# Kernel tuning notes

Hardware: AMD Instinct MI355X
Metric: run time of the kernel (lower is better)

Reference implementation:

```python
import jax, jax.numpy as jnp
import numpy as np
import math

POOL = 7          # RoIAlign output_size
SR = 2            # sampling_ratio


def _roi_align(feat, boxes, bidx):
    """torchvision RoIAlign, aligned=False, spatial_scale=1.0, sampling_ratio=2.
    feat: [B,C,H,W]; boxes: [N,4] (x1,y1,x2,y2) in pixel coords of this level;
    bidx: [N] int batch indices. Returns [N,C,POOL,POOL]."""
    B, C, H, W = feat.shape
    x1, y1, x2, y2 = boxes[:, 0], boxes[:, 1], boxes[:, 2], boxes[:, 3]
    roi_w = jnp.maximum(x2 - x1, 1.0)
    roi_h = jnp.maximum(y2 - y1, 1.0)
    bin_w = roi_w / POOL
    bin_h = roi_h / POOL
    # sample-point offsets within the ROI, in bin units: [POOL, SR]
    off = jnp.arange(POOL, dtype=feat.dtype)[:, None] + (jnp.arange(SR, dtype=feat.dtype)[None, :] + 0.5) / SR
    ys = y1[:, None, None] + bin_h[:, None, None] * off  # [N,POOL,SR]
    xs = x1[:, None, None] + bin_w[:, None, None] * off  # [N,POOL,SR]

    def prep(c, size):
        valid = (c > -1.0) & (c < size)
        c = jnp.clip(c, 0.0, size - 1)
        lo = jnp.floor(c).astype(jnp.int32)
        hi = jnp.minimum(lo + 1, size - 1)
        return lo, hi, c - lo, valid

    y_lo, y_hi, fy, vy = prep(ys, H)
    x_lo, x_hi, fx, vx = prep(xs, W)

    b = bidx.astype(jnp.int32)[:, None, None, None, None]  # [N,1,1,1,1]

    def gather(yi, xi):
        # -> [N,POOL,SR,POOL,SR,C] (advanced indices broadcast, channel slice last)
        return feat[b, :, yi[:, :, :, None, None], xi[:, None, None, :, :]]

    hy = (1.0 - fy)[:, :, :, None, None, None]
    ly = fy[:, :, :, None, None, None]
    hx = (1.0 - fx)[:, None, None, :, :, None]
    lx = fx[:, None, None, :, :, None]
    v = (gather(y_lo, x_lo) * hy * hx + gather(y_lo, x_hi) * hy * lx
         + gather(y_hi, x_lo) * ly * hx + gather(y_hi, x_hi) * ly * lx)
    valid = (vy[:, :, :, None, None] & vx[:, None, None, :, :])[..., None]
    v = jnp.where(valid, v, 0.0)
    out = v.mean(axis=(2, 4))          # average over SRxSR samples -> [N,POOL,POOL,C]
    return out.transpose(0, 3, 1, 2)   # [N,C,POOL,POOL]


def setup_inputs() -> dict:
    key = jax.random.key(0)
    k2, k3, k4, k5, kxy, kwh, kbi = jax.random.split(key, 7)
    N = 1000
    p2 = jax.random.normal(k2, (2, 256, 256, 256), dtype=jnp.float32)
    p3 = jax.random.normal(k3, (2, 256, 128, 128), dtype=jnp.float32)
    p4 = jax.random.normal(k4, (2, 256, 64, 64), dtype=jnp.float32)
    p5 = jax.random.normal(k5, (2, 256, 32, 32), dtype=jnp.float32)
    xy = jax.random.uniform(kxy, (N, 2), minval=0.0, maxval=0.7)
    wh = jax.random.uniform(kwh, (N, 2), minval=0.02, maxval=0.3)
    rpn_bbox = jnp.concatenate([xy, xy + wh], axis=1)  # (x1,y1,x2,y2) normalized
    box_index = jax.random.randint(kbi, (N,), 0, 2, dtype=jnp.int32)
    return {"p2": p2, "p3": p3, "p4": p4, "p5": p5,
            "rpn_bbox": rpn_bbox, "box_index": box_index}


def reference(p2, p3, p4, p5, rpn_bbox, box_index):
    feats = [p2, p3, p4, p5]
    N = rpn_bbox.shape[0]
    x1, y1, x2, y2 = rpn_bbox[:, 0], rpn_bbox[:, 1], rpn_bbox[:, 2], rpn_bbox[:, 3]
    area = (y2 - y1) * (x2 - x1)
    roi_level = jnp.log(jnp.sqrt(area)) / math.log(2.0)
    roi_level = jnp.clip(jnp.round(roi_level) + 4.0, 0.0, 3.0).astype(jnp.int32)
    # Compute RoIAlign of every ROI at every level, then select per-ROI level.
    # (The masked-select / per-level dispatch / argsort-combine in the original
    # restores original ROI order, so this is mathematically identical.)
    pooled_per_level = jnp.stack(
        [_roi_align(f, rpn_bbox * f.shape[3], box_index) for f in feats], axis=0
    )  # [4, N, C, 7, 7]
    pooled = pooled_per_level[roi_level, jnp.arange(N)]  # [N, C, 7, 7]
    return pooled
```

## Files before the change

### kernel.cpp

```cpp
#include <hip/hip_runtime.h>
#include <math.h>

#define POOL 7
#define NCELL 49
#define NCH 256
#define CH_SPLIT 8
#define CHPB (NCH / CH_SPLIT)
#define CHPW (CHPB / 4)
#define LDSF 640
#define NIT 10

typedef __attribute__((address_space(1))) void global_void;
typedef __attribute__((address_space(3))) void lds_void;
__device__ __forceinline__ void async_stage(const float* g, float* l) {
    __builtin_amdgcn_global_load_lds((global_void*)g, (lds_void*)l, 4, 0, 0);
}

__global__ __launch_bounds__(256, 8) void roi_align_fpn_kernel(
    const float* __restrict__ p2, const float* __restrict__ p3,
    const float* __restrict__ p4, const float* __restrict__ p5,
    const float* __restrict__ boxes, const int* __restrict__ bidx,
    float* __restrict__ out, int N)
{
    __shared__ float smem[4][2][LDSF];
    const int n = blockIdx.y;
    const int t = threadIdx.x;
    const int wave = t >> 6;
    const int lane = t & 63;

    float bx1 = boxes[4 * n + 0], by1 = boxes[4 * n + 1];
    float bx2 = boxes[4 * n + 2], by2 = boxes[4 * n + 3];
    float area = (by2 - by1) * (bx2 - bx1);
    float lvlf = logf(sqrtf(area)) * 1.4426950408889634f;
    int level = (int)fminf(fmaxf(rintf(lvlf) + 4.0f, 0.0f), 3.0f);
    int W = 256 >> level;
    int HW = W * W;
    float scale = (float)W;
    float x1 = bx1 * scale, y1 = by1 * scale;
    float bin_w = fmaxf((bx2 - bx1) * scale, 1.0f) * (1.0f / POOL);
    float bin_h = fmaxf((by2 - by1) * scale, 1.0f) * (1.0f / POOL);

    const float* feat = (level == 0) ? p2 : (level == 1) ? p3 : (level == 2) ? p4 : p5;
    feat += (size_t)bidx[n] * NCH * HW;

    float yA = y1 + bin_h * 0.25f, yB = y1 + bin_h * 6.75f;
    float xA = x1 + bin_w * 0.25f, xB = x1 + bin_w * 6.75f;
    int y0  = (int)floorf(fminf(fmaxf(yA, 0.f), (float)(W - 1)));
    int y1h = min((int)floorf(fminf(fmaxf(yB, 0.f), (float)(W - 1))) + 1, W - 1);
    int x0  = (int)floorf(fminf(fmaxf(xA, 0.f), (float)(W - 1)));
    x0 = min(x0, W - 2);
    int x1p = min((int)floorf(fminf(fmaxf(xB, 0.f), (float)(W - 1))) + 1, W - 1);
    int ww = x1p - x0 + 1;
    int wh = y1h - y0 + 1;
    wh = min(wh, LDSF / ww);
    int packed = ww * wh;

    int g_off[NIT];
#pragma unroll
    for (int k = 0; k < NIT; ++k) {
        int idx = k * 64 + lane;
        idx = (idx < packed) ? idx : 0;
        int r = idx / ww;
        int c = idx - r * ww;
        g_off[k] = (y0 + r) * W + (x0 + c);
    }

    const int ch0 = blockIdx.x * CHPB + wave * CHPW;
    const float* fbase = feat + (size_t)ch0 * HW;
    float* sm = &smem[wave][0][0];

#pragma unroll
    for (int k = 0; k < NIT; ++k) async_stage(fbase + g_off[k], sm + k * 64);

    int cell = (lane < NCELL) ? lane : (NCELL - 1);
    int py = cell / POOL, px = cell % POOL;
    int loff0[4], loff1[4];
    float w00[4], w01[4], w10[4], w11[4];
#pragma unroll
    for (int s = 0; s < 4; ++s) {
        int sy = s >> 1, sx = s & 1;
        float y = y1 + bin_h * ((float)py + ((float)sy + 0.5f) * 0.5f);
        float x = x1 + bin_w * ((float)px + ((float)sx + 0.5f) * 0.5f);
        bool v = (y > -1.f) && (y < (float)W) && (x > -1.f) && (x < (float)W);
        float yc = fminf(fmaxf(y, 0.f), (float)(W - 1));
        float xc = fminf(fmaxf(x, 0.f), (float)(W - 1));
        int ylo = (int)floorf(yc), xlo = (int)floorf(xc);
        int yhi = min(ylo + 1, W - 1);
        float fy = yc - (float)ylo, fx = xc - (float)xlo;
        float vv = v ? 0.25f : 0.f;
        int bxp = min(xlo, W - 2);
        bool in = (xlo == bxp);
        float wx0 = in ? (1.f - fx) : 0.f;
        float wx1 = in ? fx : 1.f;
        float wr0 = (1.f - fy) * vv, wr1 = fy * vv;
        loff0[s] = (ylo - y0) * ww + (bxp - x0);
        loff1[s] = (yhi - y0) * ww + (bxp - x0);
        w00[s] = wr0 * wx0; w01[s] = wr0 * wx1;
        w10[s] = wr1 * wx0; w11[s] = wr1 * wx1;
    }

    size_t obase = (size_t)n * NCH * NCELL + (size_t)ch0 * NCELL + cell;
#pragma unroll
    for (int i = 0; i < CHPW; ++i) {
        if (i + 1 < CHPW) {
            const float* fc = fbase + (size_t)(i + 1) * HW;
            float* nb = sm + ((i + 1) & 1) * LDSF;
#pragma unroll
            for (int k = 0; k < NIT; ++k) async_stage(fc + g_off[k], nb + k * 64);
            asm volatile("s_waitcnt vmcnt(10)" ::: "memory");
        } else {
            asm volatile("s_waitcnt vmcnt(0)" ::: "memory");
        }
        const float* cb = sm + (i & 1) * LDSF;
        float acc = 0.f;
#pragma unroll
        for (int s = 0; s < 4; ++s) {
            float a0 = cb[loff0[s]], a1 = cb[loff0[s] + 1];
            float b0 = cb[loff1[s]], b1 = cb[loff1[s] + 1];
            acc += w00[s] * a0 + w01[s] * a1 + w10[s] * b0 + w11[s] * b1;
        }
        if (lane < NCELL)
            __builtin_nontemporal_store(acc, out + obase + (size_t)i * NCELL);
    }
}

extern "C" void kernel_launch(void* const* d_in, const int* in_sizes, int n_in,
                              void* d_out, int out_size, void* d_ws, size_t ws_size,
                              hipStream_t stream) {
    const float* p2    = (const float*)d_in[0];
    const float* p3    = (const float*)d_in[1];
    const float* p4    = (const float*)d_in[2];
    const float* p5    = (const float*)d_in[3];
    const float* boxes = (const float*)d_in[4];
    const int*   bidx  = (const int*)d_in[5];
    float* out = (float*)d_out;
    int N = in_sizes[5];
    dim3 grid(CH_SPLIT, N);
    roi_align_fpn_kernel<<<grid, 256, 0, stream>>>(p2, p3, p4, p5, boxes, bidx, out, N);
}
```

Baseline: 274.3 us.

## Stage ROI windows with 16-byte async LDS loads on 4-aligned padded rows

```diff
diff --git a/kernel.cpp b/kernel.cpp
--- a/kernel.cpp
+++ b/kernel.cpp
@@ -8,74 +8,27 @@
 #define CHPB (NCH / CH_SPLIT)
 #define CHPW (CHPB / 4)
 #define LDSF 640
-#define NIT 10
+#define NIT_S 10
 
 typedef __attribute__((address_space(1))) void global_void;
 typedef __attribute__((address_space(3))) void lds_void;
-__device__ __forceinline__ void async_stage(const float* g, float* l) {
+__device__ __forceinline__ void stage4(const float* g, float* l) {
     __builtin_amdgcn_global_load_lds((global_void*)g, (lds_void*)l, 4, 0, 0);
 }
-
-__global__ __launch_bounds__(256, 8) void roi_align_fpn_kernel(
-    const float* __restrict__ p2, const float* __restrict__ p3,
-    const float* __restrict__ p4, const float* __restrict__ p5,
-    const float* __restrict__ boxes, const int* __restrict__ bidx,
-    float* __restrict__ out, int N)
-{
-    __shared__ float smem[4][2][LDSF];
-    const int n = blockIdx.y;
-    const int t = threadIdx.x;
-    const int wave = t >> 6;
-    const int lane = t & 63;
-
-    float bx1 = boxes[4 * n + 0], by1 = boxes[4 * n + 1];
-    float bx2 = boxes[4 * n + 2], by2 = boxes[4 * n + 3];
-    float area = (by2 - by1) * (bx2 - bx1);
-    float lvlf = logf(sqrtf(area)) * 1.4426950408889634f;
-    int level = (int)fminf(fmaxf(rintf(lvlf) + 4.0f, 0.0f), 3.0f);
-    int W = 256 >> level;
-    int HW = W * W;
-    float scale = (float)W;
-    float x1 = bx1 * scale, y1 = by1 * scale;
-    float bin_w = fmaxf((bx2 - bx1) * scale, 1.0f) * (1.0f / POOL);
-    float bin_h = fmaxf((by2 - by1) * scale, 1.0f) * (1.0f / POOL);
-
-    const float* feat = (level == 0) ? p2 : (level == 1) ? p3 : (level == 2) ? p4 : p5;
-    feat += (size_t)bidx[n] * NCH * HW;
-
-    float yA = y1 + bin_h * 0.25f, yB = y1 + bin_h * 6.75f;
-    float xA = x1 + bin_w * 0.25f, xB = x1 + bin_w * 6.75f;
-    int y0  = (int)floorf(fminf(fmaxf(yA, 0.f), (float)(W - 1)));
-    int y1h = min((int)floorf(fminf(fmaxf(yB, 0.f), (float)(W - 1))) + 1, W - 1);
-    int x0  = (int)floorf(fminf(fmaxf(xA, 0.f), (float)(W - 1)));
-    x0 = min(x0, W - 2);
-    int x1p = min((int)floorf(fminf(fmaxf(xB, 0.f), (float)(W - 1))) + 1, W - 1);
-    int ww = x1p - x0 + 1;
-    int wh = y1h - y0 + 1;
-    wh = min(wh, LDSF / ww);
-    int packed = ww * wh;
-
-    int g_off[NIT];
-#pragma unroll
-    for (int k = 0; k < NIT; ++k) {
-        int idx = k * 64 + lane;
-        idx = (idx < packed) ? idx : 0;
-        int r = idx / ww;
-        int c = idx - r * ww;
-        g_off[k] = (y0 + r) * W + (x0 + c);
-    }
-
-    const int ch0 = blockIdx.x * CHPB + wave * CHPW;
-    const float* fbase = feat + (size_t)ch0 * HW;
-    float* sm = &smem[wave][0][0];
-
-#pragma unroll
-    for (int k = 0; k < NIT; ++k) async_stage(fbase + g_off[k], sm + k * 64);
-
+__device__ __forceinline__ void stage16(const float* g, float* l) {
+    __builtin_amdgcn_global_load_lds((global_void*)g, (lds_void*)l, 16, 0, 0);
+}
+
+struct Tab {
+    int loff0[4], loff1[4];
+    float w00[4], w01[4], w10[4], w11[4];
+};
+
+__device__ __forceinline__ void make_tab(Tab& tb, int lane, int W, int rs, int xb, int y0,
+                                         float x1, float y1, float bin_w, float bin_h)
+{
     int cell = (lane < NCELL) ? lane : (NCELL - 1);
     int py = cell / POOL, px = cell % POOL;
-    int loff0[4], loff1[4];
-    float w00[4], w01[4], w10[4], w11[4];
 #pragma unroll
     for (int s = 0; s < 4; ++s) {
         int sy = s >> 1, sx = s & 1;
@@ -93,34 +46,165 @@
         float wx0 = in ? (1.f - fx) : 0.f;
         float wx1 = in ? fx : 1.f;
         float wr0 = (1.f - fy) * vv, wr1 = fy * vv;
-        loff0[s] = (ylo - y0) * ww + (bxp - x0);
-        loff1[s] = (yhi - y0) * ww + (bxp - x0);
-        w00[s] = wr0 * wx0; w01[s] = wr0 * wx1;
-        w10[s] = wr1 * wx0; w11[s] = wr1 * wx1;
-    }
-
-    size_t obase = (size_t)n * NCH * NCELL + (size_t)ch0 * NCELL + cell;
-#pragma unroll
+        tb.loff0[s] = (ylo - y0) * rs + (bxp - xb);
+        tb.loff1[s] = (yhi - y0) * rs + (bxp - xb);
+        tb.w00[s] = wr0 * wx0; tb.w01[s] = wr0 * wx1;
+        tb.w10[s] = wr1 * wx0; tb.w11[s] = wr1 * wx1;
+    }
+}
+
+__device__ __forceinline__ float consume(const float* cb, const Tab& tb)
+{
+    float acc = 0.f;
+#pragma unroll
+    for (int s = 0; s < 4; ++s) {
+        float a0 = cb[tb.loff0[s]], a1 = cb[tb.loff0[s] + 1];
+        float b0 = cb[tb.loff1[s]], b1 = cb[tb.loff1[s] + 1];
+        acc += tb.w00[s] * a0 + tb.w01[s] * a1 + tb.w10[s] * b0 + tb.w11[s] * b1;
+    }
+    return acc;
+}
+
+template <int NIT4>
+__device__ __forceinline__ void box_x4(
+    const float* fbase, float* outp, float* sm, int lane,
+    int W, int HW, int wwa, int y0, int x0a, int ngrp,
+    float x1, float y1, float bin_w, float bin_h)
+{
+    int g_off[NIT4];
+    bool act[NIT4];
+    int wwa4 = wwa >> 2;
+#pragma unroll
+    for (int k = 0; k < NIT4; ++k) {
+        int idx = k * 64 + lane;
+        act[k] = idx < ngrp;
+        int ii = act[k] ? idx : 0;
+        int r = ii / wwa4;
+        int c = ii - r * wwa4;
+        g_off[k] = (y0 + r) * W + x0a + c * 4;
+    }
+#pragma unroll
+    for (int k = 0; k < NIT4; ++k)
+        if (act[k]) stage16(fbase + g_off[k], sm + k * 256);
+
+    Tab tb;
+    make_tab(tb, lane, W, wwa, x0a, y0, x1, y1, bin_w, bin_h);
+
+#pragma unroll 2
     for (int i = 0; i < CHPW; ++i) {
         if (i + 1 < CHPW) {
             const float* fc = fbase + (size_t)(i + 1) * HW;
             float* nb = sm + ((i + 1) & 1) * LDSF;
 #pragma unroll
-            for (int k = 0; k < NIT; ++k) async_stage(fc + g_off[k], nb + k * 64);
+            for (int k = 0; k < NIT4; ++k)
+                if (act[k]) stage16(fc + g_off[k], nb + k * 256);
+            if constexpr (NIT4 == 1) asm volatile("s_waitcnt vmcnt(1)" ::: "memory");
+            else if constexpr (NIT4 == 2) asm volatile("s_waitcnt vmcnt(2)" ::: "memory");
+            else                          asm volatile("s_waitcnt vmcnt(3)" ::: "memory");
+        } else {
+            asm volatile("s_waitcnt vmcnt(0)" ::: "memory");
+        }
+        float acc = consume(sm + (i & 1) * LDSF, tb);
+        if (lane < NCELL)
+            __builtin_nontemporal_store(acc, outp + (size_t)i * NCELL);
+    }
+}
+
+__device__ __forceinline__ void box_s(
+    const float* fbase, float* outp, float* sm, int lane,
+    int W, int HW, int ww, int y0, int x0, int packed,
+    float x1, float y1, float bin_w, float bin_h)
+{
+    int g_off[NIT_S];
+#pragma unroll
+    for (int k = 0; k < NIT_S; ++k) {
+        int idx = k * 64 + lane;
+        idx = (idx < packed) ? idx : 0;
+        int r = idx / ww;
+        int c = idx - r * ww;
+        g_off[k] = (y0 + r) * W + (x0 + c);
+    }
+#pragma unroll
+    for (int k = 0; k < NIT_S; ++k) stage4(fbase + g_off[k], sm + k * 64);
+
+    Tab tb;
+    make_tab(tb, lane, W, ww, x0, y0, x1, y1, bin_w, bin_h);
+
+#pragma unroll 2
+    for (int i = 0; i < CHPW; ++i) {
+        if (i + 1 < CHPW) {
+            const float* fc = fbase + (size_t)(i + 1) * HW;
+            float* nb = sm + ((i + 1) & 1) * LDSF;
+#pragma unroll
+            for (int k = 0; k < NIT_S; ++k) stage4(fc + g_off[k], nb + k * 64);
             asm volatile("s_waitcnt vmcnt(10)" ::: "memory");
         } else {
             asm volatile("s_waitcnt vmcnt(0)" ::: "memory");
         }
-        const float* cb = sm + (i & 1) * LDSF;
-        float acc = 0.f;
-#pragma unroll
-        for (int s = 0; s < 4; ++s) {
-            float a0 = cb[loff0[s]], a1 = cb[loff0[s] + 1];
-            float b0 = cb[loff1[s]], b1 = cb[loff1[s] + 1];
-            acc += w00[s] * a0 + w01[s] * a1 + w10[s] * b0 + w11[s] * b1;
-        }
+        float acc = consume(sm + (i & 1) * LDSF, tb);
         if (lane < NCELL)
-            __builtin_nontemporal_store(acc, out + obase + (size_t)i * NCELL);
+            __builtin_nontemporal_store(acc, outp + (size_t)i * NCELL);
+    }
+}
+
+__global__ __launch_bounds__(256, 8) void roi_align_fpn_kernel(
+    const float* __restrict__ p2, const float* __restrict__ p3,
+    const float* __restrict__ p4, const float* __restrict__ p5,
+    const float* __restrict__ boxes, const int* __restrict__ bidx,
+    float* __restrict__ out, int N)
+{
+    __shared__ float smem[4][2][LDSF];
+    const int n = blockIdx.y;
+    const int t = threadIdx.x;
+    const int wave = t >> 6;
+    const int lane = t & 63;
+
+    float bx1 = boxes[4 * n + 0], by1 = boxes[4 * n + 1];
+    float bx2 = boxes[4 * n + 2], by2 = boxes[4 * n + 3];
+    float area = (by2 - by1) * (bx2 - bx1);
+    float lvlf = logf(sqrtf(area)) * 1.4426950408889634f;
+    int level = (int)fminf(fmaxf(rintf(lvlf) + 4.0f, 0.0f), 3.0f);
+    int W = 256 >> level;
+    int HW = W * W;
+    float scale = (float)W;
+    float x1 = bx1 * scale, y1 = by1 * scale;
+    float bin_w = fmaxf((bx2 - bx1) * scale, 1.0f) * (1.0f / POOL);
+    float bin_h = fmaxf((by2 - by1) * scale, 1.0f) * (1.0f / POOL);
+
+    const float* feat = (level == 0) ? p2 : (level == 1) ? p3 : (level == 2) ? p4 : p5;
+    feat += (size_t)bidx[n] * NCH * HW;
+
+    float yA = y1 + bin_h * 0.25f, yB = y1 + bin_h * 6.75f;
+    float xA = x1 + bin_w * 0.25f, xB = x1 + bin_w * 6.75f;
+    int y0  = (int)floorf(fminf(fmaxf(yA, 0.f), (float)(W - 1)));
+    int y1h = min((int)floorf(fminf(fmaxf(yB, 0.f), (float)(W - 1))) + 1, W - 1);
+    int x0  = (int)floorf(fminf(fmaxf(xA, 0.f), (float)(W - 1)));
+    x0 = min(x0, W - 2);
+    int x1p = min((int)floorf(fminf(fmaxf(xB, 0.f), (float)(W - 1))) + 1, W - 1);
+    int ww = x1p - x0 + 1;
+    int wh = y1h - y0 + 1;
+
+    int x0a = x0 & ~3;
+    int wwa = ((x1p - x0a + 1) + 3) & ~3;
+    if ((wwa & 15) == 0) wwa += 4;
+    int padded = wwa * wh;
+
+    const int ch0 = blockIdx.x * CHPB + wave * CHPW;
+    const float* fbase = feat + (size_t)ch0 * HW;
+    float* sm = &smem[wave][0][0];
+    int cell = (lane < NCELL) ? lane : (NCELL - 1);
+    float* outp = out + (size_t)n * NCH * NCELL + (size_t)ch0 * NCELL + cell;
+
+    if (padded <= LDSF) {
+        int ngrp = (wwa >> 2) * wh;
+        int nit4 = (ngrp + 63) >> 6;
+        if (nit4 == 1)      box_x4<1>(fbase, outp, sm, lane, W, HW, wwa, y0, x0a, ngrp, x1, y1, bin_w, bin_h);
+        else if (nit4 == 2) box_x4<2>(fbase, outp, sm, lane, W, HW, wwa, y0, x0a, ngrp, x1, y1, bin_w, bin_h);
+        else                box_x4<3>(fbase, outp, sm, lane, W, HW, wwa, y0, x0a, ngrp, x1, y1, bin_w, bin_h);
+    } else {
+        int whc = min(wh, LDSF / ww);
+        int packed = ww * whc;
+        box_s(fbase, outp, sm, lane, W, HW, ww, y0, x0, packed, x1, y1, bin_w, bin_h);
     }
 }
 
```

After: 274.5 us. Within noise of the previous version (+0.1%).
